# Performance work log

Measured on AMD Instinct MI355X. Metric: run time of the kernel, lower is better.

Reference implementation:

```python
import jax, jax.numpy as jnp
import numpy as np

INNER_DIM = 64
NUM_LABELS = 16
BIG_NEG = 1e12


def setup_inputs() -> dict:
    key = jax.random.key(0)
    k1, k2 = jax.random.split(key)
    B, S, H = 8, 512, 768
    sequence_output = jax.random.normal(k1, (B, S, H), dtype=jnp.float32)
    attention_mask = jnp.ones((B, S), dtype=jnp.int32)
    W = jax.random.normal(k2, (NUM_LABELS * INNER_DIM * 2, H), dtype=jnp.float32) * 0.02
    b = jnp.zeros((NUM_LABELS * INNER_DIM * 2,), dtype=jnp.float32)
    return {"sequence_output": sequence_output, "attention_mask": attention_mask,
            "W": W, "b": b}


def _rope_sincos(seq_len, dim, dtype):
    # interleaved sinusoidal embedding: [sin0,cos0,sin1,cos1,...]
    pos = jnp.arange(seq_len, dtype=dtype)[:, None]              # [S,1]
    idx = jnp.arange(dim // 2, dtype=dtype)
    theta = jnp.power(jnp.asarray(1000.0, dtype), -2.0 * idx / dim)
    ang = pos * theta                                            # [S, dim/2]
    # cos_pos/sin_pos after repeat_interleave(2): [c0,c0,c1,c1,...]
    cos_pos = jnp.repeat(jnp.cos(ang), 2, axis=-1)               # [S, dim]
    sin_pos = jnp.repeat(jnp.sin(ang), 2, axis=-1)               # [S, dim]
    return sin_pos, cos_pos


def _rotate_half_interleaved(x):
    # stack([-x[...,1::2], x[...,::2]], -1).reshape(x.shape)
    x2 = jnp.stack([-x[..., 1::2], x[..., ::2]], axis=-1)
    return x2.reshape(x.shape)


def reference(sequence_output, attention_mask, W, b):
    B, S, H = sequence_output.shape
    L, D = NUM_LABELS, INNER_DIM
    # dense projection then split into per-label q/k: [B,S,L,2D]
    out = (sequence_output @ W.T + b).reshape(B, S, L, 2 * D)
    qw, kw = out[..., :D], out[..., D:]                          # [B,S,L,D]

    sin_pos, cos_pos = _rope_sincos(S, D, sequence_output.dtype)
    cos_pos = cos_pos[None, :, None, :]                          # [1,S,1,D]
    sin_pos = sin_pos[None, :, None, :]
    qw = qw * cos_pos + _rotate_half_interleaved(qw) * sin_pos
    kw = kw * cos_pos + _rotate_half_interleaved(kw) * sin_pos

    logits = jnp.einsum('bmhd,bnhd->bhmn', qw, kw)               # [B,L,S,S]

    pad = attention_mask.astype(logits.dtype)[:, None, None, :]  # [B,1,1,S]
    logits = logits * pad - (1.0 - pad) * BIG_NEG

    tril = jnp.tril(jnp.ones((S, S), dtype=logits.dtype), -1)    # strictly lower
    logits = logits - tril * BIG_NEG
    return logits / (D ** 0.5)
```

## Files before the change

kernel.cpp:

```cpp
#include <hip/hip_runtime.h>
#include <hip/hip_bf16.h>

typedef __bf16 bf16;
typedef __attribute__((ext_vector_type(8))) __bf16 bf16x8;
typedef __attribute__((ext_vector_type(4))) float f32x4;
typedef __attribute__((ext_vector_type(4))) int i32x4;
typedef __attribute__((ext_vector_type(2))) unsigned int u32x2;
typedef __attribute__((ext_vector_type(4))) unsigned int u32x4;

#define BIG_NEG 1000000000000.0f
#define NEG_LOG_STEP 0.21586735253866545f
#define EXP_NEG_STEP 0.8058421877614818f

#define GLOAD_LDS16(g, l)                                                     \
    __builtin_amdgcn_global_load_lds(                                         \
        (const __attribute__((address_space(1))) void*)(g),                   \
        (__attribute__((address_space(3))) void*)(l), 16, 0, 0)

static __device__ inline u32x2 pack4_bf16(f32x4 v) {
    union { bf16 h[4]; u32x2 u; } t;
    t.h[0] = (bf16)v.x; t.h[1] = (bf16)v.y; t.h[2] = (bf16)v.z; t.h[3] = (bf16)v.w;
    return t.u;
}

__global__ __launch_bounds__(256) void convert_kernel(
    const float* __restrict__ X, const float* __restrict__ W,
    bf16* __restrict__ Xb, bf16* __restrict__ Wb)
{
    const int NX8 = (8 * 512 * 768) / 8;
    int idx = blockIdx.x * 256 + threadIdx.x;
    const float* src; bf16* dst; int i;
    if (idx < NX8) { src = X; dst = Xb; i = idx; }
    else           { src = W; dst = Wb; i = idx - NX8; }
    f32x4 a = __builtin_nontemporal_load(reinterpret_cast<const f32x4*>(src) + i * 2);
    f32x4 b = __builtin_nontemporal_load(reinterpret_cast<const f32x4*>(src) + i * 2 + 1);
    u32x2 lo = pack4_bf16(a), hi = pack4_bf16(b);
    u32x4 o; o.x = lo.x; o.y = lo.y; o.z = hi.x; o.w = hi.y;
    reinterpret_cast<u32x4*>(dst)[i] = o;
}

__global__ __launch_bounds__(512) void proj_rope_kernel(
    const bf16* __restrict__ A, const bf16* __restrict__ B,
    const float* __restrict__ bias,
    bf16* __restrict__ q_ws, bf16* __restrict__ k_ws)
{
    const int K = 768;
    __shared__ __align__(16) bf16 As[128][32];
    __shared__ __align__(16) bf16 Bs[128][32];

    const int tid  = threadIdx.x;
    const int lane = tid & 63;
    const int wave = tid >> 6;
    const int wr   = wave >> 2;
    const int wc   = wave & 3;
    const int brow = blockIdx.x * 128;
    const int bcol = blockIdx.y * 128;
    const int lane15 = lane & 15;
    const int kq = (lane >> 4) * 8;
    const int srow = tid >> 2;
    const int scol = (tid & 3) * 8;

    const bf16* Aaddr = A + (size_t)(brow + srow) * K + scol;
    const bf16* Baddr = B + (size_t)(bcol + srow) * K + scol;
    bf16* AsDst = &As[wave * 16][0];
    bf16* BsDst = &Bs[wave * 16][0];

    f32x4 acc[2][4] = {};

    for (int k0 = 0; k0 < K; k0 += 32) {
        GLOAD_LDS16(Aaddr + k0, AsDst);
        GLOAD_LDS16(Baddr + k0, BsDst);
        __syncthreads();

        bf16x8 af[4], bfv[2];
        #pragma unroll
        for (int mf = 0; mf < 4; ++mf)
            af[mf] = *reinterpret_cast<bf16x8*>(&As[wr * 64 + mf * 16 + lane15][kq]);
        #pragma unroll
        for (int nf = 0; nf < 2; ++nf)
            bfv[nf] = *reinterpret_cast<bf16x8*>(&Bs[wc * 32 + nf * 16 + lane15][kq]);
        #pragma unroll
        for (int nf = 0; nf < 2; ++nf)
            #pragma unroll
            for (int mf = 0; mf < 4; ++mf)
                acc[nf][mf] = __builtin_amdgcn_mfma_f32_16x16x32_bf16(
                    bfv[nf], af[mf], acc[nf][mf], 0, 0, 0);
        __syncthreads();
    }

    const int mb = brow + wr * 64 + lane15;
    const int nbase = bcol + wc * 32 + (lane >> 4) * 4;
    #pragma unroll
    for (int nf = 0; nf < 2; ++nf) {
        int n0 = nbase + nf * 16;
        int d0 = n0 & 127;
        int l  = n0 >> 7;
        int dd = d0 & 63;
        int p0 = dd >> 1;
        float th0 = __expf(-(float)p0 * NEG_LOG_STEP);
        float th1 = th0 * EXP_NEG_STEP;
        f32x4 bn = *reinterpret_cast<const f32x4*>(&bias[n0]);
        bf16* dst = (d0 < 64) ? q_ws : k_ws;
        #pragma unroll
        for (int mf = 0; mf < 4; ++mf) {
            int m = mb + mf * 16;
            int s = m & 511;
            int b = m >> 9;
            float fs = (float)s;
            f32x4 a = acc[nf][mf];
            float v0 = a.x + bn.x, v1 = a.y + bn.y;
            float v2 = a.z + bn.z, v3 = a.w + bn.w;
            float sn0, cs0, sn1, cs1;
            __sincosf(fs * th0, &sn0, &cs0);
            __sincosf(fs * th1, &sn1, &cs1);
            union { bf16 h[4]; u32x2 u; } t;
            t.h[0] = (bf16)(v0 * cs0 - v1 * sn0);
            t.h[1] = (bf16)(v1 * cs0 + v0 * sn0);
            t.h[2] = (bf16)(v2 * cs1 - v3 * sn1);
            t.h[3] = (bf16)(v3 * cs1 + v2 * sn1);
            *reinterpret_cast<u32x2*>(
                &dst[(((size_t)(b * 16 + l) * 512) + s) * 64 + dd]) = t.u;
        }
    }
}

__global__ __launch_bounds__(256) void attn_kernel(
    const bf16* __restrict__ q_ws, const bf16* __restrict__ k_ws,
    const int* __restrict__ mask, float* __restrict__ out)
{
    __shared__ __align__(16) bf16 Qs[128][72];
    __shared__ __align__(16) bf16 Ks[128][72];

    const int tid  = threadIdx.x;
    const int lane = tid & 63;
    const int wave = tid >> 6;
    const int wr   = wave >> 1;
    const int wc   = wave & 1;
    const int bl   = blockIdx.z;
    const int brow = blockIdx.x * 128;
    const int bcol = blockIdx.y * 128;
    const int b    = bl >> 4;
    const int* mrow = mask + b * 512;
    float* obase = out + (size_t)bl * 512 * 512;

    if (brow >= bcol + 128) {
        int cg = tid & 31;
        int n0 = bcol + cg * 4;
        i32x4 mi = *reinterpret_cast<const i32x4*>(&mrow[n0]);
        f32x4 o;
        o.x = (-(1.0f - (float)mi.x) * BIG_NEG - BIG_NEG) * 0.125f;
        o.y = (-(1.0f - (float)mi.y) * BIG_NEG - BIG_NEG) * 0.125f;
        o.z = (-(1.0f - (float)mi.z) * BIG_NEG - BIG_NEG) * 0.125f;
        o.w = (-(1.0f - (float)mi.w) * BIG_NEG - BIG_NEG) * 0.125f;
        int r0 = tid >> 5;
        #pragma unroll
        for (int i = 0; i < 16; ++i) {
            int row = brow + i * 8 + r0;
            __builtin_nontemporal_store(
                o, reinterpret_cast<f32x4*>(&obase[(size_t)row * 512 + n0]));
        }
        return;
    }

    const bf16* qbase = q_ws + (size_t)bl * 512 * 64;
    const bf16* kbase = k_ws + (size_t)bl * 512 * 64;
    const int lane15 = lane & 15;
    const int kq = (lane >> 4) * 8;

    #pragma unroll
    for (int pass = 0; pass < 4; ++pass) {
        int e   = (pass * 256 + tid) * 8;
        int row = e >> 6;
        int col = e & 63;
        *reinterpret_cast<u32x4*>(&Qs[row][col]) =
            *reinterpret_cast<const u32x4*>(&qbase[(size_t)(brow + row) * 64 + col]);
        *reinterpret_cast<u32x4*>(&Ks[row][col]) =
            *reinterpret_cast<const u32x4*>(&kbase[(size_t)(bcol + row) * 64 + col]);
    }
    __syncthreads();

    f32x4 acc[4][4] = {};
    #pragma unroll
    for (int ks = 0; ks < 2; ++ks) {
        bf16x8 qf[4], kf[4];
        #pragma unroll
        for (int mf = 0; mf < 4; ++mf)
            qf[mf] = *reinterpret_cast<bf16x8*>(
                &Qs[wr * 64 + mf * 16 + lane15][ks * 32 + kq]);
        #pragma unroll
        for (int nf = 0; nf < 4; ++nf)
            kf[nf] = *reinterpret_cast<bf16x8*>(
                &Ks[wc * 64 + nf * 16 + lane15][ks * 32 + kq]);
        #pragma unroll
        for (int nf = 0; nf < 4; ++nf)
            #pragma unroll
            for (int mf = 0; mf < 4; ++mf)
                acc[nf][mf] = __builtin_amdgcn_mfma_f32_16x16x32_bf16(
                    kf[nf], qf[mf], acc[nf][mf], 0, 0, 0);
    }

    const int nb = bcol + wc * 64 + (lane >> 4) * 4;
    const int mbase = brow + wr * 64 + lane15;
    #pragma unroll
    for (int nf = 0; nf < 4; ++nf) {
        int n0 = nb + nf * 16;
        i32x4 mi = *reinterpret_cast<const i32x4*>(&mrow[n0]);
        f32x4 pf; pf.x = (float)mi.x; pf.y = (float)mi.y;
        pf.z = (float)mi.z; pf.w = (float)mi.w;
        f32x4 mt;
        mt.x = (1.0f - pf.x) * BIG_NEG; mt.y = (1.0f - pf.y) * BIG_NEG;
        mt.z = (1.0f - pf.z) * BIG_NEG; mt.w = (1.0f - pf.w) * BIG_NEG;
        #pragma unroll
        for (int mf = 0; mf < 4; ++mf) {
            int m = mbase + mf * 16;
            f32x4 a = acc[nf][mf];
            f32x4 o;
            o.x = (a.x * pf.x - mt.x - ((m > n0 + 0) ? BIG_NEG : 0.0f)) * 0.125f;
            o.y = (a.y * pf.y - mt.y - ((m > n0 + 1) ? BIG_NEG : 0.0f)) * 0.125f;
            o.z = (a.z * pf.z - mt.z - ((m > n0 + 2) ? BIG_NEG : 0.0f)) * 0.125f;
            o.w = (a.w * pf.w - mt.w - ((m > n0 + 3) ? BIG_NEG : 0.0f)) * 0.125f;
            __builtin_nontemporal_store(
                o, reinterpret_cast<f32x4*>(&obase[(size_t)m * 512 + n0]));
        }
    }
}

extern "C" void kernel_launch(void* const* d_in, const int* in_sizes, int n_in,
                              void* d_out, int out_size, void* d_ws, size_t ws_size,
                              hipStream_t stream) {
    const float* X    = (const float*)d_in[0];
    const int*   mask = (const int*)d_in[1];
    const float* W    = (const float*)d_in[2];
    const float* bias = (const float*)d_in[3];

    float* out = (float*)d_out;

    bf16* q_ws = (bf16*)d_ws;
    bf16* k_ws = q_ws + (size_t)8 * 16 * 512 * 64;

    bf16* Xb = (bf16*)d_out;
    bf16* Wb = Xb + (size_t)8 * 512 * 768;

    const int NX8 = (8 * 512 * 768) / 8;
    const int NW8 = (2048 * 768) / 8;
    convert_kernel<<<(NX8 + NW8) / 256, 256, 0, stream>>>(X, W, Xb, Wb);
    proj_rope_kernel<<<dim3(32, 16), 512, 0, stream>>>(Xb, Wb, bias, q_ws, k_ws);
    attn_kernel<<<dim3(4, 4, 128), 256, 0, stream>>>(q_ws, k_ws, mask, out);
}
```

Before: 67.57 us.

## Pipeline projection GEMM with 4-buffer LDS ring and prefetch depth two

Replaces the single-buffered load/sync/compute loop in the projection GEMM with a four-slot LDS ring. Tiles are prefetched two k-steps ahead using direct global-to-LDS loads, and explicit vmcnt waits plus one barrier per iteration replace the two __syncthreads calls. The goal is to hide global load latency behind MFMA work and halve barrier count, at the cost of four times the LDS footprint, which may reduce occupancy.

```diff
diff --git a/kernel.cpp b/kernel.cpp
--- a/kernel.cpp
+++ b/kernel.cpp
@@ -45,8 +45,9 @@
     bf16* __restrict__ q_ws, bf16* __restrict__ k_ws)
 {
     const int K = 768;
-    __shared__ __align__(16) bf16 As[128][32];
-    __shared__ __align__(16) bf16 Bs[128][32];
+    const int NT = 24;
+    __shared__ __align__(16) bf16 As[4][128][32];
+    __shared__ __align__(16) bf16 Bs[4][128][32];
 
     const int tid  = threadIdx.x;
     const int lane = tid & 63;
@@ -62,31 +63,53 @@
 
     const bf16* Aaddr = A + (size_t)(brow + srow) * K + scol;
     const bf16* Baddr = B + (size_t)(bcol + srow) * K + scol;
-    bf16* AsDst = &As[wave * 16][0];
-    bf16* BsDst = &Bs[wave * 16][0];
 
     f32x4 acc[2][4] = {};
 
-    for (int k0 = 0; k0 < K; k0 += 32) {
-        GLOAD_LDS16(Aaddr + k0, AsDst);
-        GLOAD_LDS16(Baddr + k0, BsDst);
-        __syncthreads();
-
-        bf16x8 af[4], bfv[2];
-        #pragma unroll
-        for (int mf = 0; mf < 4; ++mf)
-            af[mf] = *reinterpret_cast<bf16x8*>(&As[wr * 64 + mf * 16 + lane15][kq]);
-        #pragma unroll
-        for (int nf = 0; nf < 2; ++nf)
-            bfv[nf] = *reinterpret_cast<bf16x8*>(&Bs[wc * 32 + nf * 16 + lane15][kq]);
-        #pragma unroll
-        for (int nf = 0; nf < 2; ++nf)
-            #pragma unroll
-            for (int mf = 0; mf < 4; ++mf)
-                acc[nf][mf] = __builtin_amdgcn_mfma_f32_16x16x32_bf16(
-                    bfv[nf], af[mf], acc[nf][mf], 0, 0, 0);
-        __syncthreads();
-    }
+#define STAGE(c, t)                                                            \
+    do {                                                                       \
+        GLOAD_LDS16(Aaddr + (t) * 32, &As[c][wave * 16][0]);                   \
+        GLOAD_LDS16(Baddr + (t) * 32, &Bs[c][wave * 16][0]);                   \
+    } while (0)
+
+#define COMPUTE(c)                                                             \
+    do {                                                                       \
+        bf16x8 af[4], bfv[2];                                                  \
+        _Pragma("unroll")                                                      \
+        for (int mf = 0; mf < 4; ++mf)                                         \
+            af[mf] = *reinterpret_cast<bf16x8*>(                               \
+                &As[c][wr * 64 + mf * 16 + lane15][kq]);                       \
+        _Pragma("unroll")                                                      \
+        for (int nf = 0; nf < 2; ++nf)                                         \
+            bfv[nf] = *reinterpret_cast<bf16x8*>(                              \
+                &Bs[c][wc * 32 + nf * 16 + lane15][kq]);                       \
+        _Pragma("unroll")                                                      \
+        for (int nf = 0; nf < 2; ++nf)                                         \
+            _Pragma("unroll")                                                  \
+            for (int mf = 0; mf < 4; ++mf)                                     \
+                acc[nf][mf] = __builtin_amdgcn_mfma_f32_16x16x32_bf16(         \
+                    bfv[nf], af[mf], acc[nf][mf], 0, 0, 0);                    \
+    } while (0)
+
+    STAGE(0, 0);
+    STAGE(1, 1);
+    #pragma unroll 4
+    for (int t = 0; t < NT; ++t) {
+        const int c = t & 3;
+        if (t + 2 < NT) {
+            STAGE((t + 2) & 3, t + 2);
+            asm volatile("s_waitcnt vmcnt(4)" ::: "memory");
+        } else if (t + 1 < NT) {
+            asm volatile("s_waitcnt vmcnt(2)" ::: "memory");
+        } else {
+            asm volatile("s_waitcnt vmcnt(0)" ::: "memory");
+        }
+        __builtin_amdgcn_s_barrier();
+        __builtin_amdgcn_sched_barrier(0);
+        COMPUTE(c);
+    }
+#undef STAGE
+#undef COMPUTE
 
     const int mb = brow + wr * 64 + lane15;
     const int nbase = bcol + wc * 32 + (lane >> 4) * 4;
```

New measurement: 67.54 us. No clear change (-0.0%).
